# Optimization experiments

Measured on AMD Instinct MI355X. Metric: run time of the kernel, lower is better.

Reference implementation:

```python
import jax, jax.numpy as jnp
import numpy as np
import math

# ---- module hyperparameters (from init_kwargs) ----
IN_CHANS, OUT_CHANS = 64, 64
NLAT_IN, NLON_IN = 91, 180
NLAT_OUT, NLON_OUT = 91, 180  # same resolution -> longitudinal stride 1
NR, NPHI = 5, 6               # kernel_shape
KSIZE = (NR - 1) * NPHI + 1   # 25 basis functions (1 center + (NR-1)*NPHI ring sectors)
THETA_CUTOFF = 4.0 * math.pi / float(NLAT_OUT - 1)
# latitude support window: basis vanishes for |theta_out - theta_in| > cutoff
_HALF = int(math.ceil(THETA_CUTOFF / (math.pi / (NLAT_IN - 1))))
WIN = 2 * _HALF + 1


def _precompute_psi():
    """Precompute DISCO basis tensor psi (values of the piecewise-linear
    spherical basis functions, weighted by quadrature weights), restricted to
    the latitudinal support window. Returns (psi [K,To,W,P], ti_idx [To,W])."""
    theta_in = np.pi * np.arange(NLAT_IN) / (NLAT_IN - 1)    # equiangular colatitudes
    theta_out = np.pi * np.arange(NLAT_OUT) / (NLAT_OUT - 1)
    phi_in = 2.0 * np.pi * np.arange(NLON_IN) / NLON_IN
    offs = np.arange(-_HALF, _HALF + 1)
    ti_raw = np.arange(NLAT_OUT)[:, None] + offs[None, :]    # [To, W]
    valid = (ti_raw >= 0) & (ti_raw < NLAT_IN)
    ti_idx = np.clip(ti_raw, 0, NLAT_IN - 1)
    to = theta_out[:, None, None]                            # [To,1,1]
    ti = theta_in[ti_idx][:, :, None]                        # [To,W,1]
    ph = phi_in[None, None, :]                               # [1,1,P]
    # coordinates of input point in frame where the output point (theta_out, 0)
    # is rotated to the north pole (rotation by -theta_out about y-axis)
    xx = np.cos(to) * np.sin(ti) * np.cos(ph) - np.sin(to) * np.cos(ti)
    yy = np.sin(ti) * np.sin(ph)
    zz = np.sin(to) * np.sin(ti) * np.cos(ph) + np.cos(to) * np.cos(ti)
    r = np.arccos(np.clip(zz, -1.0, 1.0))                    # great-circle distance
    phi = np.mod(np.arctan2(yy, xx), 2.0 * np.pi)            # azimuth around output point
    dr = THETA_CUTOFF / (NR - 1)
    dphi = 2.0 * np.pi / NPHI
    inside = (r <= THETA_CUTOFF) & valid[:, :, None]
    psi = np.zeros((KSIZE,) + r.shape, dtype=np.float64)
    # k = 0: isotropic center hat
    psi[0] = np.where(inside, np.maximum(0.0, 1.0 - r / dr), 0.0)
    # rings ir = 1..NR-1, azimuthal sectors ip = 0..NPHI-1 (periodic hat in phi)
    for ir in range(1, NR):
        rad = np.maximum(0.0, 1.0 - np.abs(r - ir * dr) / dr)
        for ip in range(NPHI):
            dp = np.abs(np.mod(phi - ip * dphi + np.pi, 2.0 * np.pi) - np.pi)
            ang = np.maximum(0.0, 1.0 - dp / dphi)
            psi[1 + (ir - 1) * NPHI + ip] = np.where(inside, rad * ang, 0.0)
    # fold in equiangular quadrature weights of the input grid
    quad = np.sin(theta_in) * (np.pi / (NLAT_IN - 1)) * (2.0 * np.pi / NLON_IN)
    psi = psi * quad[ti_idx][None, :, :, None]
    return jnp.asarray(psi, dtype=jnp.float32), jnp.asarray(ti_idx, dtype=jnp.int32)


PSI, TI_IDX = _precompute_psi()  # PSI: [K, To, W, P], TI_IDX: [To, W]


def setup_inputs() -> dict:
    key = jax.random.key(0)
    k1, k2 = jax.random.split(key)
    x = jax.random.normal(k1, (2, IN_CHANS, NLAT_IN, NLON_IN), dtype=jnp.float32)
    scale = 1.0 / math.sqrt(IN_CHANS * KSIZE)
    weight = scale * jax.random.normal(k2, (OUT_CHANS, IN_CHANS, KSIZE), dtype=jnp.float32)
    return {"x": x, "weight": weight}


def reference(x, weight):
    # DISCO S2 conv: out[b,o,to,q] = sum_{c,k} w[o,c,k] * sum_{ti,p} psi[k,to,ti,(p-q) mod P] * x[b,c,ti,p]
    # The longitudinal shift is a circular cross-correlation -> evaluate via rFFT.
    x = x.astype(jnp.float32)  # wrapper casts to float32 around the conv
    xw = x[:, :, TI_IDX, :]                          # [B,C,To,W,P] latitudinal gather
    Xf = jnp.fft.rfft(xw, axis=-1)                   # [B,C,To,W,F]
    Pf = jnp.fft.rfft(PSI, axis=-1)                  # [K,To,W,F]
    # correlation: FFT(z) = conj(FFT(psi)) * FFT(x), contracting the lat window
    Zf = jnp.einsum('ktwf,bctwf->bcktf', jnp.conj(Pf), Xf)   # [B,C,K,To,F]
    Of = jnp.einsum('ock,bcktf->botf', weight.astype(Zf.dtype), Zf)
    out = jnp.fft.irfft(Of, n=NLON_IN, axis=-1)      # [B,Cout,To,P]
    return out.astype(x.dtype)
```

## Files before the change

kernel.cpp:

```cpp
#include <hip/hip_runtime.h>
#include <math.h>
#include <string.h>

#define NLAT 91
#define NLON 180
#define NCH  64
#define KSZ  25
#define NW   9
#define HALF 4
#define NB   2
#define CG   4
#define CPG  16
#define THREADS 192
#define XW   360
#define EUNIT 512
#define ENT_CAP 262144
#define UCAP 1024
#define LCAP 1024

#define KOFF_OFF 0
#define KOFF_BYTES (NLAT * (KSZ + 1) * 4)
#define UNITS_OFF 9728
#define UNITS_BYTES (UCAP * 16)
#define ENTS_OFF (UNITS_OFF + UNITS_BYTES)

#ifndef M_PI
#define M_PI 3.14159265358979323846
#endif

typedef unsigned int u32;

static int build_tables(unsigned char* blob, int* ne_out)
{
#pragma clang fp contract(off)
    int* koff  = (int*)(blob + KOFF_OFF);
    u32* units = (u32*)(blob + UNITS_OFF);
    u32* ents  = (u32*)(blob + ENTS_OFF);

    static double sth[NLAT], cth[NLAT], cphv[NLON], sphv[NLON];
    for (int t = 0; t < NLAT; t++) {
        double th = (M_PI * (double)t) / 90.0;
        sth[t] = sin(th); cth[t] = cos(th);
    }
    for (int q = 0; q < NLON; q++) {
        double ph = (2.0 * M_PI * (double)q) / 180.0;
        cphv[q] = cos(ph); sphv[q] = sin(ph);
    }
    const double cutoff = (4.0 * M_PI) / 90.0;
    const double dr     = cutoff / 4.0;
    const double dphi   = (2.0 * M_PI) / 6.0;

    static int   lcnt[KSZ];
    static u32   loff_[KSZ][LCAP];
    static float lval[KSZ][LCAP];

    int ne = 0, nu = 0;
    for (int t = 0; t < NLAT; t++) {
        for (int k = 0; k < KSZ; k++) lcnt[k] = 0;
        for (int w = 0; w < NW; w++) {
            int ti_raw = t - HALF + w;
            int valid = (ti_raw >= 0) && (ti_raw < NLAT);
            int ti = ti_raw < 0 ? 0 : (ti_raw > NLAT - 1 ? NLAT - 1 : ti_raw);
            for (int q = 0; q < NLON; q++) {
                double t1 = sth[t] * sth[ti];
                double t2 = t1 * cphv[q];
                double t3 = cth[t] * cth[ti];
                double zz = t2 + t3;
                if (zz > 1.0) zz = 1.0;
                if (zz < -1.0) zz = -1.0;
                double r = acos(zz);
                if (!(valid && (r <= cutoff))) continue;
                double xx = (cth[t] * sth[ti]) * cphv[q] - sth[t] * cth[ti];
                double yy = sth[ti] * sphv[q];
                double phi = atan2(yy, xx);
                { double m = fmod(phi, 2.0 * M_PI); if (m < 0.0) m += 2.0 * M_PI; phi = m; }
                double quad = sth[ti] * (M_PI / 90.0) * ((2.0 * M_PI) / 180.0);
                int dq = (q <= 90) ? q : q - NLON;
                u32 off = (u32)(w * XW + 90 + dq);
                double v0 = fmax(0.0, 1.0 - r / dr);
                float f0 = (float)(v0 * quad);
                if (f0 != 0.f && lcnt[0] < LCAP) {
                    loff_[0][lcnt[0]] = off; lval[0][lcnt[0]] = f0; lcnt[0]++;
                }
                for (int ir = 1; ir < 5; ir++) {
                    double rad = fmax(0.0, 1.0 - fabs(r - ir * dr) / dr);
                    for (int ip = 0; ip < 6; ip++) {
                        double a = (phi - ip * dphi) + M_PI;
                        double m = fmod(a, 2.0 * M_PI);
                        if (m < 0.0) m += 2.0 * M_PI;
                        double dp = fabs(m - M_PI);
                        double ang = fmax(0.0, 1.0 - dp / dphi);
                        float f = (float)((rad * ang) * quad);
                        int k = 1 + (ir - 1) * 6 + ip;
                        if (f != 0.f && lcnt[k] < LCAP) {
                            loff_[k][lcnt[k]] = off; lval[k][lcnt[k]] = f; lcnt[k]++;
                        }
                    }
                }
            }
        }
        int tBase = ne;
        for (int k = 0; k < KSZ; k++) {
            koff[t * (KSZ + 1) + k] = ne;
            for (int i = 0; i < lcnt[k] && ne < ENT_CAP; i++) {
                ents[2 * ne] = loff_[k][i];
                ents[2 * ne + 1] = __builtin_bit_cast(u32, lval[k][i]);
                ne++;
            }
            while (((ne - koff[t * (KSZ + 1) + k]) & 7) && ne < ENT_CAP) {
                ents[2 * ne] = 0; ents[2 * ne + 1] = 0; ne++;
            }
        }
        koff[t * (KSZ + 1) + KSZ] = ne;
        for (int e0 = tBase; e0 < ne; e0 += EUNIT) {
            int e1 = e0 + EUNIT < ne ? e0 + EUNIT : ne;
            int kb = 0;
            while (kb < KSZ &&
                   !(koff[t * (KSZ + 1) + kb] <= e0 && e0 < koff[t * (KSZ + 1) + kb + 1]))
                kb++;
            if (nu < UCAP) {
                units[nu * 4 + 0] = (u32)t;
                units[nu * 4 + 1] = (u32)e0;
                units[nu * 4 + 2] = (u32)e1;
                units[nu * 4 + 3] = (u32)kb;
                nu++;
            }
        }
    }
    *ne_out = ne;
    return nu;
}

__global__ void transpose_w(const float* __restrict__ wgt, float* __restrict__ wt)
{
    int i = blockIdx.x * blockDim.x + threadIdx.x;
    if (i >= NCH * NCH * KSZ) return;
    int o = i / (NCH * KSZ);
    int rem = i - o * (NCH * KSZ);
    int c = rem / KSZ;
    int k = rem - c * KSZ;
    wt[((size_t)c * KSZ + k) * NCH + o] = wgt[i];
}

__global__ __launch_bounds__(THREADS, 4) void disco_fused(
    const float* __restrict__ x, const float* __restrict__ wt,
    const uint2* __restrict__ ents, const int* __restrict__ koffG,
    const uint4* __restrict__ units, float* __restrict__ out)
{
    uint4 u = units[blockIdx.x];
    int t = (int)u.x, eBeg = (int)u.y, eEnd = (int)u.z, kBeg = (int)u.w;
    int cg = blockIdx.y, b = blockIdx.z;
    int tid = threadIdx.x;
    int p = tid < NLON ? tid : NLON - 1;
    bool act = tid < NLON;
    __shared__ float xs[NW * XW];
    const int* ko = koffG + t * (KSZ + 1);

    float acc[NCH];
#pragma unroll
    for (int o = 0; o < NCH; o++) acc[o] = 0.f;

    for (int ci = 0; ci < CPG; ci++) {
        int c = cg * CPG + ci;
        __syncthreads();
        const float* xc = x + ((size_t)(b * NCH + c)) * (NLAT * NLON);
#pragma unroll
        for (int w = 0; w < NW; w++) {
            int tw = t - HALF + w;
            int ti = tw < 0 ? 0 : (tw > NLAT - 1 ? NLAT - 1 : tw);
            const float* xr = xc + ti * NLON;
            for (int i = tid; i < XW; i += THREADS) {
                int src = i + 90;
                if (src >= NLON) src -= NLON;
                if (src >= NLON) src -= NLON;
                xs[w * XW + i] = xr[src];
            }
        }
        __syncthreads();

        const float* xp = xs + p;
        int e = eBeg, k = kBeg;
        while (e < eEnd) {
            int kend = ko[k + 1];
            if (kend > eEnd) kend = eEnd;
            float z0 = 0.f, z1 = 0.f, z2 = 0.f, z3 = 0.f;
            for (; e < kend; e += 8) {
                uint2 a0 = ents[e + 0], a1 = ents[e + 1], a2 = ents[e + 2], a3 = ents[e + 3];
                uint2 a4 = ents[e + 4], a5 = ents[e + 5], a6 = ents[e + 6], a7 = ents[e + 7];
                z0 = fmaf(__uint_as_float(a0.y), xp[a0.x], z0);
                z1 = fmaf(__uint_as_float(a1.y), xp[a1.x], z1);
                z2 = fmaf(__uint_as_float(a2.y), xp[a2.x], z2);
                z3 = fmaf(__uint_as_float(a3.y), xp[a3.x], z3);
                z0 = fmaf(__uint_as_float(a4.y), xp[a4.x], z0);
                z1 = fmaf(__uint_as_float(a5.y), xp[a5.x], z1);
                z2 = fmaf(__uint_as_float(a6.y), xp[a6.x], z2);
                z3 = fmaf(__uint_as_float(a7.y), xp[a7.x], z3);
            }
            float zk = (z0 + z1) + (z2 + z3);
            const float* wk = wt + ((size_t)c * KSZ + k) * NCH;
#pragma unroll
            for (int o = 0; o < NCH; o++)
                acc[o] = fmaf(wk[o], zk, acc[o]);
            k++;
            if (k > KSZ) break;
        }
    }

    if (act) {
        float* op = out + ((size_t)b * NCH * NLAT * NLON) + (size_t)t * NLON + p;
#pragma unroll
        for (int o = 0; o < NCH; o++)
            atomicAdd(op + (size_t)o * (NLAT * NLON), acc[o]);
    }
}

extern "C" void kernel_launch(void* const* d_in, const int* in_sizes, int n_in,
                              void* d_out, int out_size, void* d_ws, size_t ws_size,
                              hipStream_t stream)
{
    const float* x   = (const float*)d_in[0];
    const float* wgt = (const float*)d_in[1];
    char* ws = (char*)d_ws;

    const size_t WT_BYTES = (size_t)NCH * KSZ * NCH * 4;
    float* wt = (float*)ws;
    unsigned char* d_blob = (unsigned char*)(ws + WT_BYTES);

    static unsigned char h_blob[ENTS_OFF + (size_t)ENT_CAP * 8];
    int ne = 0;
    int nu = build_tables(h_blob, &ne);
    size_t blob_bytes = (size_t)ENTS_OFF + (size_t)ne * 8;

    hipMemsetAsync(d_out, 0, (size_t)out_size * 4, stream);
    hipMemcpyAsync(d_blob, h_blob, blob_bytes, hipMemcpyHostToDevice, stream);
    transpose_w<<<(NCH * NCH * KSZ + 255) / 256, 256, 0, stream>>>(wgt, wt);

    const uint2* ents  = (const uint2*)(d_blob + ENTS_OFF);
    const int*   koffG = (const int*)(d_blob + KOFF_OFF);
    const uint4* units = (const uint4*)(d_blob + UNITS_OFF);

    disco_fused<<<dim3(nu, CG, NB), THREADS, 0, stream>>>(
        x, wt, ents, koffG, units, (float*)d_out);
}
```

Baseline: 490.1 us.

## Pack sparse basis entries into contiguous runs of four with shared base offset

```diff
diff --git a/kernel.cpp b/kernel.cpp
--- a/kernel.cpp
+++ b/kernel.cpp
@@ -9,20 +9,21 @@
 #define NW   9
 #define HALF 4
 #define NB   2
-#define CG   4
-#define CPG  16
+#define CG   8
+#define CPG  8
 #define THREADS 192
 #define XW   360
-#define EUNIT 512
-#define ENT_CAP 262144
-#define UCAP 1024
+#define XSPAD 8
+#define QUNIT 160
+#define QCAP 32768
+#define UCAP 2048
 #define LCAP 1024
 
-#define KOFF_OFF 0
-#define KOFF_BYTES (NLAT * (KSZ + 1) * 4)
-#define UNITS_OFF 9728
-#define UNITS_BYTES (UCAP * 16)
-#define ENTS_OFF (UNITS_OFF + UNITS_BYTES)
+#define KOFF_OFF   0
+#define UNITS_OFF  9728
+#define QVALS_OFF  (UNITS_OFF + UCAP * 16)
+#define QBASE_OFF  (QVALS_OFF + QCAP * 16)
+#define BLOB_MAX   (QBASE_OFF + QCAP * 4)
 
 #ifndef M_PI
 #define M_PI 3.14159265358979323846
@@ -30,12 +31,13 @@
 
 typedef unsigned int u32;
 
-static int build_tables(unsigned char* blob, int* ne_out)
+static int build_tables(unsigned char* blob, int* nq_out)
 {
 #pragma clang fp contract(off)
-    int* koff  = (int*)(blob + KOFF_OFF);
-    u32* units = (u32*)(blob + UNITS_OFF);
-    u32* ents  = (u32*)(blob + ENTS_OFF);
+    int*   koff  = (int*)(blob + KOFF_OFF);
+    u32*   units = (u32*)(blob + UNITS_OFF);
+    float* qvals = (float*)(blob + QVALS_OFF);
+    u32*   qbase = (u32*)(blob + QBASE_OFF);
 
     static double sth[NLAT], cth[NLAT], cphv[NLON], sphv[NLON];
     for (int t = 0; t < NLAT; t++) {
@@ -51,17 +53,18 @@
     const double dphi   = (2.0 * M_PI) / 6.0;
 
     static int   lcnt[KSZ];
-    static u32   loff_[KSZ][LCAP];
+    static int   loff_[KSZ][LCAP];
     static float lval[KSZ][LCAP];
 
-    int ne = 0, nu = 0;
+    int nq = 0, nu = 0;
     for (int t = 0; t < NLAT; t++) {
         for (int k = 0; k < KSZ; k++) lcnt[k] = 0;
         for (int w = 0; w < NW; w++) {
             int ti_raw = t - HALF + w;
             int valid = (ti_raw >= 0) && (ti_raw < NLAT);
             int ti = ti_raw < 0 ? 0 : (ti_raw > NLAT - 1 ? NLAT - 1 : ti_raw);
-            for (int q = 0; q < NLON; q++) {
+            for (int dq = -89; dq <= 90; dq++) {
+                int q = dq < 0 ? dq + NLON : dq;
                 double t1 = sth[t] * sth[ti];
                 double t2 = t1 * cphv[q];
                 double t3 = cth[t] * cth[ti];
@@ -75,8 +78,7 @@
                 double phi = atan2(yy, xx);
                 { double m = fmod(phi, 2.0 * M_PI); if (m < 0.0) m += 2.0 * M_PI; phi = m; }
                 double quad = sth[ti] * (M_PI / 90.0) * ((2.0 * M_PI) / 180.0);
-                int dq = (q <= 90) ? q : q - NLON;
-                u32 off = (u32)(w * XW + 90 + dq);
+                int off = w * XW + 90 + dq;
                 double v0 = fmax(0.0, 1.0 - r / dr);
                 float f0 = (float)(v0 * quad);
                 if (f0 != 0.f && lcnt[0] < LCAP) {
@@ -99,35 +101,52 @@
                 }
             }
         }
-        int tBase = ne;
+        int tQ = nq;
         for (int k = 0; k < KSZ; k++) {
-            koff[t * (KSZ + 1) + k] = ne;
-            for (int i = 0; i < lcnt[k] && ne < ENT_CAP; i++) {
-                ents[2 * ne] = loff_[k][i];
-                ents[2 * ne + 1] = __builtin_bit_cast(u32, lval[k][i]);
-                ne++;
-            }
-            while (((ne - koff[t * (KSZ + 1) + k]) & 7) && ne < ENT_CAP) {
-                ents[2 * ne] = 0; ents[2 * ne + 1] = 0; ne++;
-            }
-        }
-        koff[t * (KSZ + 1) + KSZ] = ne;
-        for (int e0 = tBase; e0 < ne; e0 += EUNIT) {
-            int e1 = e0 + EUNIT < ne ? e0 + EUNIT : ne;
+            koff[t * (KSZ + 1) + k] = nq;
+            int i = 0;
+            while (i < lcnt[k] && nq < QCAP) {
+                int j = i;
+                while (j + 1 < lcnt[k] && loff_[k][j + 1] == loff_[k][j] + 1) j++;
+                int L = j - i + 1;
+                int full = L / 4, rem = L - 4 * full;
+                for (int f = 0; f < full && nq < QCAP; f++) {
+                    qbase[nq] = (u32)loff_[k][i + 4 * f];
+                    for (int s = 0; s < 4; s++) qvals[4 * nq + s] = lval[k][i + 4 * f + s];
+                    nq++;
+                }
+                if (rem && nq < QCAP) {
+                    if (L >= 4) {
+                        qbase[nq] = (u32)(loff_[k][i] + L - 4);
+                        for (int s = 0; s < 4; s++)
+                            qvals[4 * nq + s] = (s >= 4 - rem) ? lval[k][i + L - 4 + s] : 0.f;
+                    } else {
+                        qbase[nq] = (u32)loff_[k][i];
+                        for (int s = 0; s < 4; s++)
+                            qvals[4 * nq + s] = (s < rem) ? lval[k][i + s] : 0.f;
+                    }
+                    nq++;
+                }
+                i = j + 1;
+            }
+        }
+        koff[t * (KSZ + 1) + KSZ] = nq;
+        for (int q0 = tQ; q0 < nq; q0 += QUNIT) {
+            int q1 = q0 + QUNIT < nq ? q0 + QUNIT : nq;
             int kb = 0;
             while (kb < KSZ &&
-                   !(koff[t * (KSZ + 1) + kb] <= e0 && e0 < koff[t * (KSZ + 1) + kb + 1]))
+                   !(koff[t * (KSZ + 1) + kb] <= q0 && q0 < koff[t * (KSZ + 1) + kb + 1]))
                 kb++;
             if (nu < UCAP) {
                 units[nu * 4 + 0] = (u32)t;
-                units[nu * 4 + 1] = (u32)e0;
-                units[nu * 4 + 2] = (u32)e1;
+                units[nu * 4 + 1] = (u32)q0;
+                units[nu * 4 + 2] = (u32)q1;
                 units[nu * 4 + 3] = (u32)kb;
                 nu++;
             }
         }
     }
-    *ne_out = ne;
+    *nq_out = nq;
     return nu;
 }
 
@@ -144,16 +163,21 @@
 
 __global__ __launch_bounds__(THREADS, 4) void disco_fused(
     const float* __restrict__ x, const float* __restrict__ wt,
-    const uint2* __restrict__ ents, const int* __restrict__ koffG,
-    const uint4* __restrict__ units, float* __restrict__ out)
-{
-    uint4 u = units[blockIdx.x];
-    int t = (int)u.x, eBeg = (int)u.y, eEnd = (int)u.z, kBeg = (int)u.w;
+    const u32* __restrict__ qbase, const float4* __restrict__ qvals,
+    const int* __restrict__ koffG, const uint4* __restrict__ units,
+    float* __restrict__ out)
+{
+    uint4 uu = units[blockIdx.x];
+    int t    = __builtin_amdgcn_readfirstlane((int)uu.x);
+    int qBeg = __builtin_amdgcn_readfirstlane((int)uu.y);
+    int qEnd = __builtin_amdgcn_readfirstlane((int)uu.z);
+    int kBeg = __builtin_amdgcn_readfirstlane((int)uu.w);
     int cg = blockIdx.y, b = blockIdx.z;
     int tid = threadIdx.x;
     int p = tid < NLON ? tid : NLON - 1;
     bool act = tid < NLON;
-    __shared__ float xs[NW * XW];
+
+    __shared__ float xs[NW * XW + XSPAD];
     const int* ko = koffG + t * (KSZ + 1);
 
     float acc[NCH];
@@ -176,25 +200,23 @@
                 xs[w * XW + i] = xr[src];
             }
         }
+        if (tid < XSPAD) xs[NW * XW + tid] = 0.f;
         __syncthreads();
 
         const float* xp = xs + p;
-        int e = eBeg, k = kBeg;
-        while (e < eEnd) {
+        int e = qBeg, k = kBeg;
+        while (e < qEnd) {
             int kend = ko[k + 1];
-            if (kend > eEnd) kend = eEnd;
+            if (kend > qEnd) kend = qEnd;
             float z0 = 0.f, z1 = 0.f, z2 = 0.f, z3 = 0.f;
-            for (; e < kend; e += 8) {
-                uint2 a0 = ents[e + 0], a1 = ents[e + 1], a2 = ents[e + 2], a3 = ents[e + 3];
-                uint2 a4 = ents[e + 4], a5 = ents[e + 5], a6 = ents[e + 6], a7 = ents[e + 7];
-                z0 = fmaf(__uint_as_float(a0.y), xp[a0.x], z0);
-                z1 = fmaf(__uint_as_float(a1.y), xp[a1.x], z1);
-                z2 = fmaf(__uint_as_float(a2.y), xp[a2.x], z2);
-                z3 = fmaf(__uint_as_float(a3.y), xp[a3.x], z3);
-                z0 = fmaf(__uint_as_float(a4.y), xp[a4.x], z0);
-                z1 = fmaf(__uint_as_float(a5.y), xp[a5.x], z1);
-                z2 = fmaf(__uint_as_float(a6.y), xp[a6.x], z2);
-                z3 = fmaf(__uint_as_float(a7.y), xp[a7.x], z3);
+            for (; e < kend; ++e) {
+                int base = (int)qbase[e];
+                float4 pv = qvals[e];
+                const float* xq = xp + base;
+                z0 = fmaf(pv.x, xq[0], z0);
+                z1 = fmaf(pv.y, xq[1], z1);
+                z2 = fmaf(pv.z, xq[2], z2);
+                z3 = fmaf(pv.w, xq[3], z3);
             }
             float zk = (z0 + z1) + (z2 + z3);
             const float* wk = wt + ((size_t)c * KSZ + k) * NCH;
@@ -202,7 +224,7 @@
             for (int o = 0; o < NCH; o++)
                 acc[o] = fmaf(wk[o], zk, acc[o]);
             k++;
-            if (k > KSZ) break;
+            if (k >= KSZ) break;
         }
     }
 
@@ -226,19 +248,20 @@
     float* wt = (float*)ws;
     unsigned char* d_blob = (unsigned char*)(ws + WT_BYTES);
 
-    static unsigned char h_blob[ENTS_OFF + (size_t)ENT_CAP * 8];
-    int ne = 0;
-    int nu = build_tables(h_blob, &ne);
-    size_t blob_bytes = (size_t)ENTS_OFF + (size_t)ne * 8;
+    static unsigned char h_blob[BLOB_MAX];
+    int nq = 0;
+    int nu = build_tables(h_blob, &nq);
+    size_t blob_bytes = (size_t)QBASE_OFF + (size_t)nq * 4;
 
     hipMemsetAsync(d_out, 0, (size_t)out_size * 4, stream);
     hipMemcpyAsync(d_blob, h_blob, blob_bytes, hipMemcpyHostToDevice, stream);
     transpose_w<<<(NCH * NCH * KSZ + 255) / 256, 256, 0, stream>>>(wgt, wt);
 
-    const uint2* ents  = (const uint2*)(d_blob + ENTS_OFF);
-    const int*   koffG = (const int*)(d_blob + KOFF_OFF);
-    const uint4* units = (const uint4*)(d_blob + UNITS_OFF);
+    const u32*    qbaseD = (const u32*)(d_blob + QBASE_OFF);
+    const float4* qvalsD = (const float4*)(d_blob + QVALS_OFF);
+    const int*    koffD  = (const int*)(d_blob + KOFF_OFF);
+    const uint4*  unitsD = (const uint4*)(d_blob + UNITS_OFF);
 
     disco_fused<<<dim3(nu, CG, NB), THREADS, 0, stream>>>(
-        x, wt, ents, koffG, units, (float*)d_out);
-}
+        x, wt, qbaseD, qvalsD, koffD, unitsD, (float*)d_out);
+}
```

Result: slower. 684.2 us (+39.6%).

## Pack input channels into float4, trim shared-memory window, build tables once

Applied to the files above, without the earlier changes.

```diff
diff --git a/kernel.cpp b/kernel.cpp
--- a/kernel.cpp
+++ b/kernel.cpp
@@ -9,20 +9,21 @@
 #define NW   9
 #define HALF 4
 #define NB   2
-#define CG   4
-#define CPG  16
+#define NPK  16
+#define CG   8
+#define PPB  (NPK / CG)
 #define THREADS 192
-#define XW   360
-#define EUNIT 512
-#define ENT_CAP 262144
-#define UCAP 1024
-#define LCAP 1024
-
-#define KOFF_OFF 0
-#define KOFF_BYTES (NLAT * (KSZ + 1) * 4)
-#define UNITS_OFF 9728
-#define UNITS_BYTES (UCAP * 16)
-#define ENTS_OFF (UNITS_OFF + UNITS_BYTES)
+#define EUNIT 384
+#define ECAP  131072
+#define UCAP  512
+#define XSCAP 2560
+#define LCAP  1024
+
+#define KOFF_OFF  0
+#define ROW_OFF   9472
+#define UNITS_OFF 22784
+#define ENTS_OFF  30976
+#define BLOB_MAX  (ENTS_OFF + (size_t)ECAP * 8)
 
 #ifndef M_PI
 #define M_PI 3.14159265358979323846
@@ -33,9 +34,10 @@
 static int build_tables(unsigned char* blob, int* ne_out)
 {
 #pragma clang fp contract(off)
-    int* koff  = (int*)(blob + KOFF_OFF);
-    u32* units = (u32*)(blob + UNITS_OFF);
-    u32* ents  = (u32*)(blob + ENTS_OFF);
+    int*  koff  = (int*)(blob + KOFF_OFF);
+    int4* rowi  = (int4*)(blob + ROW_OFF);
+    u32*  units = (u32*)(blob + UNITS_OFF);
+    u32*  ents  = (u32*)(blob + ENTS_OFF);
 
     static double sth[NLAT], cth[NLAT], cphv[NLON], sphv[NLON];
     for (int t = 0; t < NLAT; t++) {
@@ -51,17 +53,20 @@
     const double dphi   = (2.0 * M_PI) / 6.0;
 
     static int   lcnt[KSZ];
-    static u32   loff_[KSZ][LCAP];
+    static int   loff_[KSZ][LCAP];
     static float lval[KSZ][LCAP];
 
     int ne = 0, nu = 0;
     for (int t = 0; t < NLAT; t++) {
         for (int k = 0; k < KSZ; k++) lcnt[k] = 0;
+        int dqmin[NW], dqmax[NW];
+        for (int w = 0; w < NW; w++) { dqmin[w] = 999; dqmax[w] = -999; }
         for (int w = 0; w < NW; w++) {
             int ti_raw = t - HALF + w;
             int valid = (ti_raw >= 0) && (ti_raw < NLAT);
             int ti = ti_raw < 0 ? 0 : (ti_raw > NLAT - 1 ? NLAT - 1 : ti_raw);
-            for (int q = 0; q < NLON; q++) {
+            for (int dq = -89; dq <= 90; dq++) {
+                int q = dq < 0 ? dq + NLON : dq;
                 double t1 = sth[t] * sth[ti];
                 double t2 = t1 * cphv[q];
                 double t3 = cth[t] * cth[ti];
@@ -70,17 +75,18 @@
                 if (zz < -1.0) zz = -1.0;
                 double r = acos(zz);
                 if (!(valid && (r <= cutoff))) continue;
+                if (dq < dqmin[w]) dqmin[w] = dq;
+                if (dq > dqmax[w]) dqmax[w] = dq;
                 double xx = (cth[t] * sth[ti]) * cphv[q] - sth[t] * cth[ti];
                 double yy = sth[ti] * sphv[q];
                 double phi = atan2(yy, xx);
                 { double m = fmod(phi, 2.0 * M_PI); if (m < 0.0) m += 2.0 * M_PI; phi = m; }
                 double quad = sth[ti] * (M_PI / 90.0) * ((2.0 * M_PI) / 180.0);
-                int dq = (q <= 90) ? q : q - NLON;
-                u32 off = (u32)(w * XW + 90 + dq);
                 double v0 = fmax(0.0, 1.0 - r / dr);
                 float f0 = (float)(v0 * quad);
+                int pid = w * 512 + (dq + 128);
                 if (f0 != 0.f && lcnt[0] < LCAP) {
-                    loff_[0][lcnt[0]] = off; lval[0][lcnt[0]] = f0; lcnt[0]++;
+                    loff_[0][lcnt[0]] = pid; lval[0][lcnt[0]] = f0; lcnt[0]++;
                 }
                 for (int ir = 1; ir < 5; ir++) {
                     double rad = fmax(0.0, 1.0 - fabs(r - ir * dr) / dr);
@@ -93,21 +99,36 @@
                         float f = (float)((rad * ang) * quad);
                         int k = 1 + (ir - 1) * 6 + ip;
                         if (f != 0.f && lcnt[k] < LCAP) {
-                            loff_[k][lcnt[k]] = off; lval[k][lcnt[k]] = f; lcnt[k]++;
+                            loff_[k][lcnt[k]] = pid; lval[k][lcnt[k]] = f; lcnt[k]++;
                         }
                     }
                 }
             }
         }
+        int rb = 0, base[NW];
+        for (int w = 0; w < NW; w++) {
+            int len = (dqmin[w] <= dqmax[w]) ? (NLON + dqmax[w] - dqmin[w]) : 0;
+            if (rb + len > XSCAP) len = XSCAP - rb;
+            int tw = t - HALF + w;
+            int ti = tw < 0 ? 0 : (tw > NLAT - 1 ? NLAT - 1 : tw);
+            base[w] = rb;
+            rowi[t * NW + w] = make_int4(rb, len, (dqmin[w] <= dqmax[w]) ? dqmin[w] : 0, ti);
+            rb += len;
+        }
         int tBase = ne;
         for (int k = 0; k < KSZ; k++) {
             koff[t * (KSZ + 1) + k] = ne;
-            for (int i = 0; i < lcnt[k] && ne < ENT_CAP; i++) {
-                ents[2 * ne] = loff_[k][i];
-                ents[2 * ne + 1] = __builtin_bit_cast(u32, lval[k][i]);
+            for (int i = 0; i < lcnt[k] && ne < ECAP; i++) {
+                int pid = loff_[k][i];
+                int w = pid >> 9, dq = (pid & 511) - 128;
+                u32 off = (u32)(base[w] + (dq - rowi[t * NW + w].z));
+                ents[2 * ne] = off;
+                float fv = lval[k][i];
+                u32 fb; memcpy(&fb, &fv, 4);
+                ents[2 * ne + 1] = fb;
                 ne++;
             }
-            while (((ne - koff[t * (KSZ + 1) + k]) & 7) && ne < ENT_CAP) {
+            while (((ne - koff[t * (KSZ + 1) + k]) & 3) && ne < ECAP) {
                 ents[2 * ne] = 0; ents[2 * ne + 1] = 0; ne++;
             }
         }
@@ -131,78 +152,138 @@
     return nu;
 }
 
-__global__ void transpose_w(const float* __restrict__ wgt, float* __restrict__ wt)
+struct GInit {
+    unsigned char* blob;
+    int nu, ne;
+    size_t bytes;
+    GInit() {
+        static unsigned char storage[BLOB_MAX];
+        nu = build_tables(storage, &ne);
+        bytes = ENTS_OFF + (size_t)ne * 8;
+        unsigned char* p = nullptr;
+        if (hipHostMalloc((void**)&p, bytes) == hipSuccess && p) {
+            memcpy(p, storage, bytes);
+            blob = p;
+        } else {
+            blob = storage;
+        }
+    }
+};
+static GInit g_init;
+
+__global__ __launch_bounds__(THREADS) void pack_x(const float* __restrict__ x,
+                                                  float4* __restrict__ xp4)
+{
+    int t = blockIdx.x, cp = blockIdx.y, b = blockIdx.z;
+    int p = threadIdx.x;
+    if (p >= NLON) return;
+    int c0 = cp * 4;
+    float4 v;
+    v.x = x[((size_t)(b * NCH + c0 + 0) * NLAT + t) * NLON + p];
+    v.y = x[((size_t)(b * NCH + c0 + 1) * NLAT + t) * NLON + p];
+    v.z = x[((size_t)(b * NCH + c0 + 2) * NLAT + t) * NLON + p];
+    v.w = x[((size_t)(b * NCH + c0 + 3) * NLAT + t) * NLON + p];
+    xp4[((size_t)(b * NPK + cp) * NLAT + t) * NLON + p] = v;
+}
+
+__global__ void pack_w(const float* __restrict__ wgt, float4* __restrict__ wt2)
 {
     int i = blockIdx.x * blockDim.x + threadIdx.x;
-    if (i >= NCH * NCH * KSZ) return;
-    int o = i / (NCH * KSZ);
-    int rem = i - o * (NCH * KSZ);
-    int c = rem / KSZ;
-    int k = rem - c * KSZ;
-    wt[((size_t)c * KSZ + k) * NCH + o] = wgt[i];
-}
-
-__global__ __launch_bounds__(THREADS, 4) void disco_fused(
-    const float* __restrict__ x, const float* __restrict__ wt,
+    if (i >= NPK * KSZ * NCH) return;
+    int cp = i / (KSZ * NCH);
+    int rem = i - cp * (KSZ * NCH);
+    int k = rem / NCH;
+    int o = rem - k * NCH;
+    float4 v;
+    v.x = wgt[((size_t)o * NCH + cp * 4 + 0) * KSZ + k];
+    v.y = wgt[((size_t)o * NCH + cp * 4 + 1) * KSZ + k];
+    v.z = wgt[((size_t)o * NCH + cp * 4 + 2) * KSZ + k];
+    v.w = wgt[((size_t)o * NCH + cp * 4 + 3) * KSZ + k];
+    wt2[i] = v;
+}
+
+__global__ __launch_bounds__(THREADS, 3) void disco_fused(
+    const float4* __restrict__ xp4, const float4* __restrict__ wt2,
     const uint2* __restrict__ ents, const int* __restrict__ koffG,
-    const uint4* __restrict__ units, float* __restrict__ out)
-{
-    uint4 u = units[blockIdx.x];
-    int t = (int)u.x, eBeg = (int)u.y, eEnd = (int)u.z, kBeg = (int)u.w;
+    const int4* __restrict__ rowinfoG, const uint4* __restrict__ units,
+    float* __restrict__ out)
+{
+    uint4 uu = units[blockIdx.x];
+    int t    = __builtin_amdgcn_readfirstlane((int)uu.x);
+    int eBeg = __builtin_amdgcn_readfirstlane((int)uu.y);
+    int eEnd = __builtin_amdgcn_readfirstlane((int)uu.z);
+    int kBeg = __builtin_amdgcn_readfirstlane((int)uu.w);
+    if (eBeg >= eEnd) return;
     int cg = blockIdx.y, b = blockIdx.z;
     int tid = threadIdx.x;
     int p = tid < NLON ? tid : NLON - 1;
     bool act = tid < NLON;
-    __shared__ float xs[NW * XW];
+
+    __shared__ float4 xs[XSCAP];
     const int* ko = koffG + t * (KSZ + 1);
+    const int4* ri9 = rowinfoG + t * NW;
 
     float acc[NCH];
 #pragma unroll
     for (int o = 0; o < NCH; o++) acc[o] = 0.f;
 
-    for (int ci = 0; ci < CPG; ci++) {
-        int c = cg * CPG + ci;
+    for (int pk = 0; pk < PPB; pk++) {
+        int cp = cg * PPB + pk;
         __syncthreads();
-        const float* xc = x + ((size_t)(b * NCH + c)) * (NLAT * NLON);
 #pragma unroll
         for (int w = 0; w < NW; w++) {
-            int tw = t - HALF + w;
-            int ti = tw < 0 ? 0 : (tw > NLAT - 1 ? NLAT - 1 : tw);
-            const float* xr = xc + ti * NLON;
-            for (int i = tid; i < XW; i += THREADS) {
-                int src = i + 90;
-                if (src >= NLON) src -= NLON;
-                if (src >= NLON) src -= NLON;
-                xs[w * XW + i] = xr[src];
+            int4 ri = ri9[w];
+            const float4* src = xp4 + ((size_t)(b * NPK + cp) * NLAT + ri.w) * NLON;
+            for (int j = tid; j < ri.y; j += THREADS) {
+                int s = j + ri.z;
+                if (s < 0) s += NLON;
+                if (s >= NLON) s -= NLON;
+                xs[ri.x + j] = src[s];
             }
         }
         __syncthreads();
 
-        const float* xp = xs + p;
         int e = eBeg, k = kBeg;
         while (e < eEnd) {
             int kend = ko[k + 1];
             if (kend > eEnd) kend = eEnd;
-            float z0 = 0.f, z1 = 0.f, z2 = 0.f, z3 = 0.f;
-            for (; e < kend; e += 8) {
-                uint2 a0 = ents[e + 0], a1 = ents[e + 1], a2 = ents[e + 2], a3 = ents[e + 3];
-                uint2 a4 = ents[e + 4], a5 = ents[e + 5], a6 = ents[e + 6], a7 = ents[e + 7];
-                z0 = fmaf(__uint_as_float(a0.y), xp[a0.x], z0);
-                z1 = fmaf(__uint_as_float(a1.y), xp[a1.x], z1);
-                z2 = fmaf(__uint_as_float(a2.y), xp[a2.x], z2);
-                z3 = fmaf(__uint_as_float(a3.y), xp[a3.x], z3);
-                z0 = fmaf(__uint_as_float(a4.y), xp[a4.x], z0);
-                z1 = fmaf(__uint_as_float(a5.y), xp[a5.x], z1);
-                z2 = fmaf(__uint_as_float(a6.y), xp[a6.x], z2);
-                z3 = fmaf(__uint_as_float(a7.y), xp[a7.x], z3);
-            }
-            float zk = (z0 + z1) + (z2 + z3);
-            const float* wk = wt + ((size_t)c * KSZ + k) * NCH;
+            if (kend > e) {
+                float z00=0.f,z01=0.f,z02=0.f,z03=0.f;
+                float z10=0.f,z11=0.f,z12=0.f,z13=0.f;
+                float z20=0.f,z21=0.f,z22=0.f,z23=0.f;
+                float z30=0.f,z31=0.f,z32=0.f,z33=0.f;
+                for (; e < kend; e += 4) {
+                    const uint4* e4 = (const uint4*)(ents + e);
+                    uint4 A = e4[0], B = e4[1];
+                    float4 x0 = xs[A.x + p];
+                    float4 x1 = xs[A.z + p];
+                    float4 x2 = xs[B.x + p];
+                    float4 x3 = xs[B.z + p];
+                    float v0 = __uint_as_float(A.y), v1 = __uint_as_float(A.w);
+                    float v2 = __uint_as_float(B.y), v3 = __uint_as_float(B.w);
+                    z00 = fmaf(v0, x0.x, z00); z01 = fmaf(v0, x0.y, z01);
+                    z02 = fmaf(v0, x0.z, z02); z03 = fmaf(v0, x0.w, z03);
+                    z10 = fmaf(v1, x1.x, z10); z11 = fmaf(v1, x1.y, z11);
+                    z12 = fmaf(v1, x1.z, z12); z13 = fmaf(v1, x1.w, z13);
+                    z20 = fmaf(v2, x2.x, z20); z21 = fmaf(v2, x2.y, z21);
+                    z22 = fmaf(v2, x2.z, z22); z23 = fmaf(v2, x2.w, z23);
+                    z30 = fmaf(v3, x3.x, z30); z31 = fmaf(v3, x3.y, z31);
+                    z32 = fmaf(v3, x3.z, z32); z33 = fmaf(v3, x3.w, z33);
+                }
+                float zc0 = (z00 + z10) + (z20 + z30);
+                float zc1 = (z01 + z11) + (z21 + z31);
+                float zc2 = (z02 + z12) + (z22 + z32);
+                float zc3 = (z03 + z13) + (z23 + z33);
+                const float4* wk = wt2 + ((size_t)cp * KSZ + k) * NCH;
 #pragma unroll
-            for (int o = 0; o < NCH; o++)
-                acc[o] = fmaf(wk[o], zk, acc[o]);
+                for (int o = 0; o < NCH; o++) {
+                    float4 w4 = wk[o];
+                    acc[o] = fmaf(w4.w, zc3, fmaf(w4.z, zc2,
+                             fmaf(w4.y, zc1, fmaf(w4.x, zc0, acc[o]))));
+                }
+            }
             k++;
-            if (k > KSZ) break;
+            if (k >= KSZ) break;
         }
     }
 
@@ -222,23 +303,26 @@
     const float* wgt = (const float*)d_in[1];
     char* ws = (char*)d_ws;
 
-    const size_t WT_BYTES = (size_t)NCH * KSZ * NCH * 4;
-    float* wt = (float*)ws;
-    unsigned char* d_blob = (unsigned char*)(ws + WT_BYTES);
-
-    static unsigned char h_blob[ENTS_OFF + (size_t)ENT_CAP * 8];
-    int ne = 0;
-    int nu = build_tables(h_blob, &ne);
-    size_t blob_bytes = (size_t)ENTS_OFF + (size_t)ne * 8;
-
+    size_t cur = 0;
+    auto alloc = [&](size_t bytes) { size_t o = cur; cur = (cur + bytes + 255) & ~(size_t)255; return o; };
+    size_t blob_off = alloc(BLOB_MAX);
+    size_t xp4_off  = alloc((size_t)NB * NPK * NLAT * NLON * 16);
+    size_t wt2_off  = alloc((size_t)NPK * KSZ * NCH * 16);
+
+    unsigned char* d_blob = (unsigned char*)(ws + blob_off);
+    float4*        xp4    = (float4*)(ws + xp4_off);
+    float4*        wt2    = (float4*)(ws + wt2_off);
+
+    hipMemcpyAsync(d_blob, g_init.blob, g_init.bytes, hipMemcpyHostToDevice, stream);
+    pack_x<<<dim3(NLAT, NPK, NB), THREADS, 0, stream>>>(x, xp4);
+    pack_w<<<(NPK * KSZ * NCH + 255) / 256, 256, 0, stream>>>(wgt, wt2);
     hipMemsetAsync(d_out, 0, (size_t)out_size * 4, stream);
-    hipMemcpyAsync(d_blob, h_blob, blob_bytes, hipMemcpyHostToDevice, stream);
-    transpose_w<<<(NCH * NCH * KSZ + 255) / 256, 256, 0, stream>>>(wgt, wt);
-
-    const uint2* ents  = (const uint2*)(d_blob + ENTS_OFF);
-    const int*   koffG = (const int*)(d_blob + KOFF_OFF);
-    const uint4* units = (const uint4*)(d_blob + UNITS_OFF);
-
-    disco_fused<<<dim3(nu, CG, NB), THREADS, 0, stream>>>(
-        x, wt, ents, koffG, units, (float*)d_out);
-}
+
+    const uint2* entsD = (const uint2*)(d_blob + ENTS_OFF);
+    const int*   koffD = (const int*)(d_blob + KOFF_OFF);
+    const int4*  rowD  = (const int4*)(d_blob + ROW_OFF);
+    const uint4* unitD = (const uint4*)(d_blob + UNITS_OFF);
+
+    disco_fused<<<dim3(g_init.nu, CG, NB), THREADS, 0, stream>>>(
+        xp4, wt2, entsD, koffD, rowD, unitD, (float*)d_out);
+}
```

Result: faster. 407.0 us (-17.0%).
